# Kernel optimization log

Hardware: AMD Instinct MI355X
Metric: run time of the kernel (lower is better)

## Reference

```python
import jax, jax.numpy as jnp
import numpy as np

B, H, S, D = 1, 32, 2048, 128
LAST_Q = 64      # MInference uses the last 64 queries to estimate the pattern
V_TOPK = 256     # top vertical columns kept per head
S_TOPK = 512     # top slash diagonals kept per head
N_SINK = 4       # vertical columns always kept (attention sink)
N_LOCAL = 64     # local diagonals always kept
SCALE = 1.0 / np.sqrt(D)


def setup_inputs() -> dict:
    key = jax.random.key(0)
    k1, k2, k3 = jax.random.split(key, 3)
    q = jax.random.normal(k1, (B, H, S, D), jnp.float32)
    k = jax.random.normal(k2, (B, H, S, D), jnp.float32)
    v = jax.random.normal(k3, (B, H, S, D), jnp.float32)
    return {"q": q, "k": k, "v": v}


def _vertical_slash_masks(q, k):
    """Estimate per-head vertical/slash importance from the last LAST_Q queries
    and return boolean column mask [B,H,S] and diagonal mask [B,H,S]."""
    ql = q[:, :, -LAST_Q:, :]                                   # [B,H,LQ,D]
    est = jnp.einsum('bhqd,bhkd->bhqk', ql, k) * SCALE          # [B,H,LQ,S]
    rows = jnp.arange(S - LAST_Q, S)                            # global row ids
    cols = jnp.arange(S)
    causal = rows[:, None] >= cols[None, :]                     # [LQ,S]
    est = jnp.where(causal, est, -jnp.inf)
    p = jax.nn.softmax(est, axis=-1)                            # [B,H,LQ,S]

    # vertical importance: column sums of estimated attention
    vertical = p.sum(axis=2)                                    # [B,H,S]

    # slash importance: sums along diagonals d = row - col (d in [0, S-1])
    diag = jnp.clip(rows[:, None] - cols[None, :], 0, S - 1)    # negatives are causally masked (p=0)
    flat_d = diag.reshape(-1)
    flat_p = p.reshape(B * H, LAST_Q * S)
    slash = jax.vmap(lambda pr: jax.ops.segment_sum(pr, flat_d, num_segments=S))(flat_p)
    slash = slash.reshape(B, H, S)                              # [B,H,S]

    # always keep sink columns and the local diagonal band
    vertical = vertical.at[..., :N_SINK].set(jnp.inf)
    slash = slash.at[..., :N_LOCAL].set(jnp.inf)

    _, v_idx = jax.lax.top_k(vertical, V_TOPK)                  # [B,H,V_TOPK]
    _, s_idx = jax.lax.top_k(slash, S_TOPK)                     # [B,H,S_TOPK]

    scatter_true = jax.vmap(jax.vmap(lambda m, i: m.at[i].set(True)))
    vmask = scatter_true(jnp.zeros((B, H, S), bool), v_idx)     # which columns kept
    smask = scatter_true(jnp.zeros((B, H, S), bool), s_idx)     # which diagonals kept
    return vmask, smask


def reference(q, k, v):
    vmask, smask = _vertical_slash_masks(q, k)

    rows = jnp.arange(S)
    cols = jnp.arange(S)
    causal = rows[:, None] >= cols[None, :]                     # [S,S]
    d = jnp.clip(rows[:, None] - cols[None, :], 0, S - 1)       # [S,S] diagonal id

    # keep (r,c) if causal AND (column c is a top vertical OR diagonal r-c is a top slash)
    keep = causal[None, None] & (vmask[:, :, None, :] | jnp.take(smask, d, axis=-1))

    scores = jnp.einsum('bhqd,bhkd->bhqk', q, k) * SCALE        # [B,H,S,S]
    scores = jnp.where(keep, scores, -jnp.inf)
    probs = jax.nn.softmax(scores, axis=-1)                     # every row keeps diagonal 0 -> no all-masked rows
    return jnp.einsum('bhqk,bhkd->bhqd', probs, v)
```

## Files before the change

### kernel.cpp

```cpp
#include <hip/hip_runtime.h>
#include <hip/hip_bf16.h>

#define S_LEN 2048
#define NH 32
#define D_DIM 128
#define LAST_Q 64
#define SCALE_F 0.08838834764831845f
#define QSCALE (0.08838834764831845f * 1.4426950408889634f)
#define RESCALE_THR 11.54f

typedef __attribute__((ext_vector_type(8))) short bf16x8;
typedef __attribute__((ext_vector_type(4))) float f32x4;
typedef unsigned long long u64;
typedef unsigned int u32;
typedef unsigned short u16;

static __device__ __forceinline__ u16 f32_bf16(float f) {
  u32 u = __float_as_uint(f);
  u32 r = (u + 0x7FFFu + ((u >> 16) & 1u)) >> 16;
  return (u16)r;
}

static __device__ __forceinline__ u32 cvt_pk_bf16(float lo, float hi) {
  u32 r;
  asm("v_cvt_pk_bf16_f32 %0, %1, %2" : "=v"(r) : "v"(lo), "v"(hi));
  return r;
}

__global__ __launch_bounds__(256) void conv_kernel(const float* __restrict__ k,
                                                   const float* __restrict__ v,
                                                   u16* __restrict__ kpre,
                                                   u16* __restrict__ vpre) {
  int bid = blockIdx.x;
  int t = bid & 31, h = bid >> 5;
  int tid = threadIdx.x;
  int c0 = t * 64;
  __shared__ u16 Vb[64][136];
  for (int i = tid; i < 512; i += 256) {
    int r = i >> 3, s = i & 7;
    const float* srcp = v + ((size_t)(h * S_LEN + c0 + r)) * D_DIM + s * 16;
    float4 f0 = *(const float4*)(srcp);
    float4 f1 = *(const float4*)(srcp + 4);
    float4 f2 = *(const float4*)(srcp + 8);
    float4 f3 = *(const float4*)(srcp + 12);
    bf16x8 t0, t1;
    t0[0] = (short)f32_bf16(f0.x); t0[1] = (short)f32_bf16(f0.y);
    t0[2] = (short)f32_bf16(f0.z); t0[3] = (short)f32_bf16(f0.w);
    t0[4] = (short)f32_bf16(f1.x); t0[5] = (short)f32_bf16(f1.y);
    t0[6] = (short)f32_bf16(f1.z); t0[7] = (short)f32_bf16(f1.w);
    t1[0] = (short)f32_bf16(f2.x); t1[1] = (short)f32_bf16(f2.y);
    t1[2] = (short)f32_bf16(f2.z); t1[3] = (short)f32_bf16(f2.w);
    t1[4] = (short)f32_bf16(f3.x); t1[5] = (short)f32_bf16(f3.y);
    t1[6] = (short)f32_bf16(f3.z); t1[7] = (short)f32_bf16(f3.w);
    *(bf16x8*)&Vb[r][s * 16] = t0;
    *(bf16x8*)&Vb[r][s * 16 + 8] = t1;
  }
  u16* kp = kpre + (size_t)h * 262144 + (size_t)t * 8192;
#pragma unroll
  for (int j = 0; j < 4; ++j) {
    int p = j * 256 + tid;
    int r = p >> 4;
    int g = (p & 15) ^ (r & 15);
    const float* srcp = k + ((size_t)(h * S_LEN + c0 + r)) * D_DIM + g * 8;
    float4 a = *(const float4*)srcp;
    float4 b = *(const float4*)(srcp + 4);
    bf16x8 o;
    o[0] = (short)f32_bf16(a.x); o[1] = (short)f32_bf16(a.y);
    o[2] = (short)f32_bf16(a.z); o[3] = (short)f32_bf16(a.w);
    o[4] = (short)f32_bf16(b.x); o[5] = (short)f32_bf16(b.y);
    o[6] = (short)f32_bf16(b.z); o[7] = (short)f32_bf16(b.w);
    *(bf16x8*)(kp + p * 8) = o;
  }
  __syncthreads();
  u16* vp = vpre + (size_t)h * 262144 + (size_t)t * 8192;
#pragma unroll
  for (int j = 0; j < 4; ++j) {
    int p = j * 256 + tid;
    int d = p >> 3;
    int cb = (p & 7) ^ (d & 7);
    bf16x8 g;
#pragma unroll
    for (int e = 0; e < 8; ++e) g[e] = (short)Vb[cb * 8 + e][d];
    *(bf16x8*)(vp + p * 8) = g;
  }
}

__global__ __launch_bounds__(256) void est_kernel(const float* __restrict__ q,
                                                  const float* __restrict__ k,
                                                  float* __restrict__ scores) {
  int cc = blockIdx.x;
  int h = blockIdx.y;
  int tid = threadIdx.x;
  int ty = tid >> 4, tx = tid & 15;
  __shared__ float Qs[64][36];
  __shared__ float Ks[64][36];
  float acc[4][4];
#pragma unroll
  for (int i = 0; i < 4; ++i)
#pragma unroll
    for (int j = 0; j < 4; ++j) acc[i][j] = 0.f;
  const float* qbase = q + ((size_t)h * S_LEN + (S_LEN - LAST_Q)) * D_DIM;
  const float* kbase = k + ((size_t)h * S_LEN + cc * 64) * D_DIM;
  for (int dc = 0; dc < 4; ++dc) {
    __syncthreads();
    for (int i = tid; i < 512; i += 256) {
      int r = i >> 3, s = i & 7;
      float4 a = *(const float4*)(qbase + (size_t)r * D_DIM + dc * 32 + s * 4);
      *(float4*)&Qs[r][s * 4] = a;
      float4 b = *(const float4*)(kbase + (size_t)r * D_DIM + dc * 32 + s * 4);
      *(float4*)&Ks[r][s * 4] = b;
    }
    __syncthreads();
#pragma unroll
    for (int d4 = 0; d4 < 8; ++d4) {
      float4 qv[4], kv[4];
#pragma unroll
      for (int i = 0; i < 4; ++i) qv[i] = *(const float4*)&Qs[ty + 16 * i][d4 * 4];
#pragma unroll
      for (int j = 0; j < 4; ++j) kv[j] = *(const float4*)&Ks[tx + 16 * j][d4 * 4];
#pragma unroll
      for (int i = 0; i < 4; ++i)
#pragma unroll
        for (int j = 0; j < 4; ++j)
          acc[i][j] += qv[i].x * kv[j].x + qv[i].y * kv[j].y + qv[i].z * kv[j].z + qv[i].w * kv[j].w;
    }
  }
#pragma unroll
  for (int i = 0; i < 4; ++i) {
    int rl = ty + 16 * i;
    int rg = (S_LEN - LAST_Q) + rl;
#pragma unroll
    for (int j = 0; j < 4; ++j) {
      int cg = cc * 64 + tx + 16 * j;
      float vv = (cg <= rg) ? acc[i][j] * SCALE_F : -1e30f;
      scores[((size_t)h * LAST_Q + rl) * S_LEN + cg] = vv;
    }
  }
}

__global__ __launch_bounds__(256) void soft_partial_kernel(const float* __restrict__ scores,
                                                           float* __restrict__ part) {
  int h = blockIdx.x, rg = blockIdx.y;
  int tid = threadIdx.x;
  int wave = tid >> 6, lane = tid & 63;
  __shared__ float vs[2048];
  __shared__ float ss[2048];
  __shared__ float red[4];
  int i0 = tid * 8;
#pragma unroll
  for (int e = 0; e < 8; ++e) { vs[i0 + e] = 0.f; ss[i0 + e] = 0.f; }
  for (int rr = 0; rr < 8; ++rr) {
    int r = rg * 8 + rr;
    const float* sp = scores + ((size_t)h * LAST_Q + r) * S_LEN;
    float4 a = *(const float4*)(sp + i0);
    float4 b = *(const float4*)(sp + i0 + 4);
    float x[8] = {a.x, a.y, a.z, a.w, b.x, b.y, b.z, b.w};
    float wm = -1e30f;
#pragma unroll
    for (int e = 0; e < 8; ++e) wm = fmaxf(wm, x[e]);
#pragma unroll
    for (int mk = 1; mk < 64; mk <<= 1) wm = fmaxf(wm, __shfl_xor(wm, mk, 64));
    __syncthreads();
    if (lane == 0) red[wave] = wm;
    __syncthreads();
    float m = fmaxf(fmaxf(red[0], red[1]), fmaxf(red[2], red[3]));
    float psum = 0.f;
#pragma unroll
    for (int e = 0; e < 8; ++e) { x[e] = __expf(x[e] - m); psum += x[e]; }
#pragma unroll
    for (int mk = 1; mk < 64; mk <<= 1) psum += __shfl_xor(psum, mk, 64);
    __syncthreads();
    if (lane == 0) red[wave] = psum;
    __syncthreads();
    float inv = 1.f / (red[0] + red[1] + red[2] + red[3]);
    int rgl = (S_LEN - LAST_Q) + r;
#pragma unroll
    for (int e = 0; e < 8; ++e) {
      float p = x[e] * inv;
      int i = i0 + e;
      vs[i] += p;
      int d = rgl - i;
      if (d >= 0) ss[d] += p;
    }
  }
  __syncthreads();
  float* pb = part + ((size_t)(h * 8 + rg)) * 4096;
#pragma unroll
  for (int e = 0; e < 8; ++e) { pb[i0 + e] = vs[i0 + e]; pb[2048 + i0 + e] = ss[i0 + e]; }
}

__global__ __launch_bounds__(256) void topk_kernel(const float* __restrict__ part,
                                                   u64* __restrict__ vbits,
                                                   u64* __restrict__ sbits) {
  int h = blockIdx.x;
  int which = blockIdx.y;
  u64* dst = which ? (sbits + h * 32) : (vbits + h * 32);
  u32 K = which ? 512u : 256u;
  int ninf = which ? 64 : 4;
  int tid = threadIdx.x;
  int lane = tid & 63, wid = tid >> 6;
  __shared__ u32 keys[2048];
  __shared__ u32 hist[256];
  __shared__ u32 wpart[4];
  __shared__ u32 sh_pref, sh_kth;
  __shared__ u64 mbw[32];
  int i0 = tid * 8;
  float accv[8] = {0.f, 0.f, 0.f, 0.f, 0.f, 0.f, 0.f, 0.f};
  for (int rg = 0; rg < 8; ++rg) {
    const float* pp = part + ((size_t)(h * 8 + rg)) * 4096 + which * 2048 + i0;
    float4 a = *(const float4*)pp;
    float4 b = *(const float4*)(pp + 4);
    accv[0] += a.x; accv[1] += a.y; accv[2] += a.z; accv[3] += a.w;
    accv[4] += b.x; accv[5] += b.y; accv[6] += b.z; accv[7] += b.w;
  }
#pragma unroll
  for (int e = 0; e < 8; ++e) {
    int i = i0 + e;
    keys[i] = (i < ninf) ? 0x7F800000u : __float_as_uint(accv[e]);
  }
  __syncthreads();
  u32 prefix = 0;
  u32 kth = K;
  for (int shift = 24; shift >= 0; shift -= 8) {
    hist[tid] = 0;
    __syncthreads();
#pragma unroll
    for (int e = 0; e < 8; ++e) {
      u32 kk = keys[i0 + e];
      if (shift == 24 || (kk >> (shift + 8)) == (prefix >> (shift + 8)))
        atomicAdd(&hist[(kk >> shift) & 255], 1u);
    }
    __syncthreads();
    u32 v = hist[tid];
    u32 x = v;
#pragma unroll
    for (int off = 1; off < 64; off <<= 1) {
      u32 o = __shfl_up(x, off, 64);
      if (lane >= off) x += o;
    }
    if (lane == 63) wpart[wid] = x;
    __syncthreads();
    u32 base = 0;
    for (int w2 = 0; w2 < wid; ++w2) base += wpart[w2];
    u32 T = wpart[0] + wpart[1] + wpart[2] + wpart[3];
    u32 Pincl = x + base;
    u32 Sb = T - Pincl + v;
    u32 Sn = T - Pincl;
    if (Sb >= kth && Sn < kth) {
      sh_pref = prefix | ((u32)tid << shift);
      sh_kth = kth - Sn;
    }
    __syncthreads();
    prefix = sh_pref;
    kth = sh_kth;
    __syncthreads();
  }
  u32 t = prefix;
  u32 cnt = 0;
#pragma unroll
  for (int e = 0; e < 8; ++e) cnt += (keys[i0 + e] == t) ? 1u : 0u;
  u32 x = cnt;
#pragma unroll
  for (int off = 1; off < 64; off <<= 1) {
    u32 o = __shfl_up(x, off, 64);
    if (lane >= off) x += o;
  }
  if (lane == 63) wpart[wid] = x;
  __syncthreads();
  u32 base = 0;
  for (int w2 = 0; w2 < wid; ++w2) base += wpart[w2];
  u32 exc = x + base - cnt;
  unsigned char myb = 0;
  u32 seen = 0;
#pragma unroll
  for (int e = 0; e < 8; ++e) {
    u32 kk = keys[i0 + e];
    bool in = (kk > t) || (kk == t && (exc + seen) < kth);
    if (kk == t) ++seen;
    myb |= (in ? 1u : 0u) << e;
  }
  ((unsigned char*)mbw)[tid] = myb;
  __syncthreads();
  if (tid < 32) dst[tid] = mbw[tid];
}

template <bool PRE>
__global__ __launch_bounds__(256, 4) void attn_kernel(const float* __restrict__ q,
                                                      const float* __restrict__ kk,
                                                      const float* __restrict__ vv,
                                                      const u16* __restrict__ kpre,
                                                      const u16* __restrict__ vpre,
                                                      const u64* __restrict__ vbits,
                                                      const u64* __restrict__ sbits,
                                                      float* __restrict__ out) {
  int bid = blockIdx.x;
  int u = bid & 255, s = bid >> 8;
  int h = u & 31;
  int v_ = u >> 5;
  int qt;
  switch (s) {
    case 0: qt = v_; break;
    case 1: qt = 31 - v_; break;
    case 2: qt = v_ + 16; break;
    default: qt = 15 - v_; break;
  }
  int tid = threadIdx.x;
  int wave = tid >> 6, lane = tid & 63;
  int grp = lane >> 4, ln = lane & 15;

  __shared__ u16 Ks[8192];
  __shared__ u16 Vt[8192];
  __shared__ u64 smp[34];

  if (tid < 34) smp[tid] = (tid == 0 || tid == 33) ? 0ull : sbits[h * 32 + tid - 1];

  int q0w = qt * 64 + wave * 16;
  bf16x8 qf[4];
  const float* qrow = q + ((size_t)h * S_LEN + q0w + ln) * D_DIM;
#pragma unroll
  for (int ks = 0; ks < 4; ++ks) {
    const float* p = qrow + ks * 32 + grp * 8;
    float4 a = *(const float4*)p;
    float4 b = *(const float4*)(p + 4);
    bf16x8 f;
    f[0] = (short)f32_bf16(a.x * QSCALE); f[1] = (short)f32_bf16(a.y * QSCALE);
    f[2] = (short)f32_bf16(a.z * QSCALE); f[3] = (short)f32_bf16(a.w * QSCALE);
    f[4] = (short)f32_bf16(b.x * QSCALE); f[5] = (short)f32_bf16(b.y * QSCALE);
    f[6] = (short)f32_bf16(b.z * QSCALE); f[7] = (short)f32_bf16(b.w * QSCALE);
    qf[ks] = f;
  }
  f32x4 of[8];
#pragma unroll
  for (int i = 0; i < 8; ++i) of[i] = (f32x4){0.f, 0.f, 0.f, 0.f};
  float mr = -1e30f;
  float ls = 0.f;

  const int kb0 = (ln << 7) + (((0 + grp) ^ ln) << 3);
  const int kb1 = (ln << 7) + (((4 + grp) ^ ln) << 3);
  const int kb2 = (ln << 7) + (((8 + grp) ^ ln) << 3);
  const int kb3 = (ln << 7) + (((12 + grp) ^ ln) << 3);
  const int vb0 = (ln << 6) + (((0 + grp) ^ (ln & 7)) << 3);
  const int vb1 = (ln << 6) + (((4 + grp) ^ (ln & 7)) << 3);

  const u16* kp = kpre + (size_t)h * 262144;
  const u16* vp = vpre + (size_t)h * 262144;
  const float* kfb = kk + (size_t)h * S_LEN * D_DIM;
  const float* vfb = vv + (size_t)h * S_LEN * D_DIM;
  const u64* vwp = vbits + h * 32;
  int nt = qt + 1;
  int sb_lane = (lane & 48) + ((lane & 48) >> 2);

  auto dma_k = [&](int t) {
    const u16* ksrc = kp + (size_t)t * 8192;
#pragma unroll
    for (int i = 0; i < 4; ++i) {
      int chunk = wave * 4 + i;
      __builtin_amdgcn_global_load_lds(
          (const __attribute__((address_space(1))) u32*)(const void*)(ksrc + (size_t)(chunk * 64 + lane) * 8),
          (__attribute__((address_space(3))) u32*)(void*)(&Ks[chunk * 512]), 16, 0, 0);
    }
  };
  auto dma_v = [&](int t) {
    const u16* vsrc = vp + (size_t)t * 8192;
#pragma unroll
    for (int i = 0; i < 4; ++i) {
      int chunk = wave * 4 + i;
      __builtin_amdgcn_global_load_lds(
          (const __attribute__((address_space(1))) u32*)(const void*)(vsrc + (size_t)(chunk * 64 + lane) * 8),
          (__attribute__((address_space(3))) u32*)(void*)(&Vt[chunk * 512]), 16, 0, 0);
    }
  };

  if constexpr (PRE) { dma_k(0); dma_v(0); }
  __syncthreads();

  for (int t = 0; t < nt; ++t) {
    int c0 = t * 64;
    if constexpr (!PRE) {
      for (int i = tid; i < 512; i += 256) {
        int r = i >> 3, s2 = i & 7;
        const float* srcp = kfb + (size_t)(c0 + r) * D_DIM + s2 * 16;
        float4 f0 = *(const float4*)(srcp);
        float4 f1 = *(const float4*)(srcp + 4);
        float4 f2 = *(const float4*)(srcp + 8);
        float4 f3 = *(const float4*)(srcp + 12);
        bf16x8 t0, t1;
        t0[0] = (short)f32_bf16(f0.x); t0[1] = (short)f32_bf16(f0.y);
        t0[2] = (short)f32_bf16(f0.z); t0[3] = (short)f32_bf16(f0.w);
        t0[4] = (short)f32_bf16(f1.x); t0[5] = (short)f32_bf16(f1.y);
        t0[6] = (short)f32_bf16(f1.z); t0[7] = (short)f32_bf16(f1.w);
        t1[0] = (short)f32_bf16(f2.x); t1[1] = (short)f32_bf16(f2.y);
        t1[2] = (short)f32_bf16(f2.z); t1[3] = (short)f32_bf16(f2.w);
        t1[4] = (short)f32_bf16(f3.x); t1[5] = (short)f32_bf16(f3.y);
        t1[6] = (short)f32_bf16(f3.z); t1[7] = (short)f32_bf16(f3.w);
        int cb0 = s2 * 2, cb1 = s2 * 2 + 1;
        *(bf16x8*)&Ks[r * 128 + ((cb0 ^ (r & 15)) << 3)] = t0;
        *(bf16x8*)&Ks[r * 128 + ((cb1 ^ (r & 15)) << 3)] = t1;
      }
      for (int i = tid; i < 512; i += 256) {
        int r = i >> 3, s2 = i & 7;
        const float* srcp = vfb + (size_t)(c0 + r) * D_DIM + s2 * 16;
#pragma unroll
        for (int x = 0; x < 16; x += 4) {
          float4 f4 = *(const float4*)(srcp + x);
          int d0 = s2 * 16 + x;
          float vals[4] = {f4.x, f4.y, f4.z, f4.w};
#pragma unroll
          for (int y = 0; y < 4; ++y) {
            int d = d0 + y;
            Vt[d * 64 + (((r >> 3) ^ (d & 7)) << 3) + (r & 7)] = f32_bf16(vals[y]);
          }
        }
      }
      __syncthreads();
    }

    f32x4 sfr[4];
#pragma unroll
    for (int nb = 0; nb < 4; ++nb) {
      f32x4 acc = (f32x4){0.f, 0.f, 0.f, 0.f};
      acc = __builtin_amdgcn_mfma_f32_16x16x32_bf16(*(const bf16x8*)&Ks[kb0 + nb * 2048], qf[0], acc, 0, 0, 0);
      acc = __builtin_amdgcn_mfma_f32_16x16x32_bf16(*(const bf16x8*)&Ks[kb1 + nb * 2048], qf[1], acc, 0, 0, 0);
      acc = __builtin_amdgcn_mfma_f32_16x16x32_bf16(*(const bf16x8*)&Ks[kb2 + nb * 2048], qf[2], acc, 0, 0, 0);
      acc = __builtin_amdgcn_mfma_f32_16x16x32_bf16(*(const bf16x8*)&Ks[kb3 + nb * 2048], qf[3], acc, 0, 0, 0);
      sfr[nb] = acc;
    }

    float tm = sfr[0][0];
#pragma unroll
    for (int nb = 0; nb < 4; ++nb)
#pragma unroll
      for (int jj = 0; jj < 4; ++jj) tm = fmaxf(tm, sfr[nb][jj]);
    tm = fmaxf(tm, __shfl_xor(tm, 16, 64));
    tm = fmaxf(tm, __shfl_xor(tm, 32, 64));

    if (__any(tm - mr > RESCALE_THR)) {
      float mn = fmaxf(mr, tm);
      float ex = __builtin_amdgcn_exp2f(mr - mn);
      mr = mn;
      ls *= ex;
      float e0 = __shfl(ex, sb_lane, 64);
      float e1 = __shfl(ex, sb_lane + 1, 64);
      float e2 = __shfl(ex, sb_lane + 2, 64);
      float e3 = __shfl(ex, sb_lane + 3, 64);
#pragma unroll
      for (int db = 0; db < 8; ++db) {
        of[db][0] *= e0; of[db][1] *= e1; of[db][2] *= e2; of[db][3] *= e3;
      }
    }

    int Cb = (q0w + ln) - c0 - (grp << 2);
    float rs = 0.f;
    u32 pkw[8];
    if (c0 >= q0w - 48) {
#pragma unroll
      for (int nb = 0; nb < 4; ++nb) {
        float pv[4];
#pragma unroll
        for (int jj = 0; jj < 4; ++jj) {
          bool keep = (16 * nb + jj) <= Cb;
          float p = keep ? __builtin_amdgcn_exp2f(sfr[nb][jj] - mr) : 0.f;
          rs += p;
          pv[jj] = p;
        }
        pkw[nb * 2] = cvt_pk_bf16(pv[0], pv[1]);
        pkw[nb * 2 + 1] = cvt_pk_bf16(pv[2], pv[3]);
      }
    } else {
      int b0 = Cb - 63;
      int w0i = (b0 >> 6) + 1;
      int sh = b0 & 63;
      u64 lo = smp[w0i];
      u64 hi = smp[w0i + 1];
      u64 W = (sh == 0) ? lo : ((lo >> sh) | (hi << (64 - sh)));
      u64 vword = vwp[t];
#pragma unroll
      for (int nb = 0; nb < 4; ++nb) {
        u32 vn = (u32)(vword >> (16 * nb + 4 * grp)) & 0xFu;
        u32 sn = (u32)(W >> (60 - 16 * nb)) & 0xFu;
        float pv[4];
#pragma unroll
        for (int jj = 0; jj < 4; ++jj) {
          u32 keep = ((vn >> jj) | (sn >> (3 - jj))) & 1u;
          float p = keep ? __builtin_amdgcn_exp2f(sfr[nb][jj] - mr) : 0.f;
          rs += p;
          pv[jj] = p;
        }
        pkw[nb * 2] = cvt_pk_bf16(pv[0], pv[1]);
        pkw[nb * 2 + 1] = cvt_pk_bf16(pv[2], pv[3]);
      }
    }
    rs += __shfl_xor(rs, 16, 64);
    rs += __shfl_xor(rs, 32, 64);
    ls += rs;

    if constexpr (PRE) {
      __builtin_amdgcn_sched_barrier(0);
      asm volatile("s_waitcnt vmcnt(0)" ::: "memory");
      __builtin_amdgcn_s_barrier();
      if (t + 1 < nt) dma_k(t + 1);
    }

#pragma unroll
    for (int ks2 = 0; ks2 < 2; ++ks2) {
      int sl0 = ln + ((lane & 16) << 1);
      int sl1 = sl0 + 16;
      u32 a0 = __shfl(pkw[ks2 * 4 + 0], sl0, 64);
      u32 a1 = __shfl(pkw[ks2 * 4 + 1], sl0, 64);
      u32 a2 = __shfl(pkw[ks2 * 4 + 0], sl1, 64);
      u32 a3 = __shfl(pkw[ks2 * 4 + 1], sl1, 64);
      u32 b0_ = __shfl(pkw[ks2 * 4 + 2], sl0, 64);
      u32 b1_ = __shfl(pkw[ks2 * 4 + 3], sl0, 64);
      u32 b2_ = __shfl(pkw[ks2 * 4 + 2], sl1, 64);
      u32 b3_ = __shfl(pkw[ks2 * 4 + 3], sl1, 64);
      bool hi2 = grp >= 2;
      union { u32 w[4]; bf16x8 v; } pu;
      pu.w[0] = hi2 ? b0_ : a0;
      pu.w[1] = hi2 ? b1_ : a1;
      pu.w[2] = hi2 ? b2_ : a2;
      pu.w[3] = hi2 ? b3_ : a3;
      int vb = ks2 ? vb1 : vb0;
#pragma unroll
      for (int db = 0; db < 8; ++db) {
        bf16x8 vf = *(const bf16x8*)&Vt[vb + db * 1024];
        of[db] = __builtin_amdgcn_mfma_f32_16x16x32_bf16(pu.v, vf, of[db], 0, 0, 0);
      }
    }

    if constexpr (PRE) {
      __builtin_amdgcn_sched_barrier(0);
      __builtin_amdgcn_s_barrier();
      if (t + 1 < nt) {
        dma_v(t + 1);
        asm volatile("s_waitcnt vmcnt(4)" ::: "memory");
      }
      __builtin_amdgcn_s_barrier();
    } else {
      __syncthreads();
    }
  }

  float invl = 1.f / ls;
  float i0 = __shfl(invl, sb_lane, 64);
  float i1 = __shfl(invl, sb_lane + 1, 64);
  float i2 = __shfl(invl, sb_lane + 2, 64);
  float i3 = __shfl(invl, sb_lane + 3, 64);
  float* ob = out + ((size_t)h * S_LEN + q0w) * D_DIM;
#pragma unroll
  for (int db = 0; db < 8; ++db) {
    ob[(size_t)(grp * 4 + 0) * D_DIM + db * 16 + ln] = of[db][0] * i0;
    ob[(size_t)(grp * 4 + 1) * D_DIM + db * 16 + ln] = of[db][1] * i1;
    ob[(size_t)(grp * 4 + 2) * D_DIM + db * 16 + ln] = of[db][2] * i2;
    ob[(size_t)(grp * 4 + 3) * D_DIM + db * 16 + ln] = of[db][3] * i3;
  }
}

extern "C" void kernel_launch(void* const* d_in, const int* in_sizes, int n_in,
                              void* d_out, int out_size, void* d_ws, size_t ws_size,
                              hipStream_t stream) {
  const float* q = (const float*)d_in[0];
  const float* k = (const float*)d_in[1];
  const float* v = (const float*)d_in[2];
  float* out = (float*)d_out;
  float* scores = out;
  float* part = out + 4194304;
  u64* vbits = (u64*)d_ws;
  u64* sbits = vbits + 1024;
  const size_t PRE_NEED = 16384 + 2ull * 16777216;
  bool pre = ws_size >= PRE_NEED;
  u16* kpre = (u16*)((char*)d_ws + 16384);
  u16* vpre = kpre + 8388608;

  if (pre) conv_kernel<<<1024, 256, 0, stream>>>(k, v, kpre, vpre);
  est_kernel<<<dim3(32, 32), 256, 0, stream>>>(q, k, scores);
  soft_partial_kernel<<<dim3(32, 8), 256, 0, stream>>>(scores, part);
  topk_kernel<<<dim3(32, 2), 256, 0, stream>>>(part, vbits, sbits);
  if (pre)
    attn_kernel<true><<<1024, 256, 0, stream>>>(q, k, v, kpre, vpre, vbits, sbits, out);
  else
    attn_kernel<false><<<1024, 256, 0, stream>>>(q, k, v, kpre, vpre, vbits, sbits, out);
}
```

Measured before the change: 140.9 us.

## Pair causal query tiles per block, fuse conversion with estimation, split softmax partials

The attention kernel now gives each block two query tiles (qt and 31-qt). Each K/V tile staged in shared memory is used by both, which halves the block count and balances causal work across blocks. Conversion and estimation are merged into one launch by interleaving block roles. The softmax-partial kernel uses 16 row groups instead of 8 for more parallelism, and top-k reduces the extra partials. Occupancy hints drop to 2 blocks per CU because of the doubled register state (two accumulators and two Q fragments), and setprio hints are added around the MFMA sections.

```diff
diff --git a/kernel.cpp b/kernel.cpp
--- a/kernel.cpp
+++ b/kernel.cpp
@@ -27,61 +27,114 @@
   return r;
 }
 
-__global__ __launch_bounds__(256) void conv_kernel(const float* __restrict__ k,
-                                                   const float* __restrict__ v,
-                                                   u16* __restrict__ kpre,
-                                                   u16* __restrict__ vpre) {
+__global__ __launch_bounds__(256) void conv_est_kernel(const float* __restrict__ k,
+                                                       const float* __restrict__ v,
+                                                       const float* __restrict__ q,
+                                                       u16* __restrict__ kpre,
+                                                       u16* __restrict__ vpre,
+                                                       float* __restrict__ scores) {
+  __shared__ char smem[18432];
   int bid = blockIdx.x;
-  int t = bid & 31, h = bid >> 5;
+  int b = bid >> 1;
   int tid = threadIdx.x;
-  int c0 = t * 64;
-  __shared__ u16 Vb[64][136];
-  for (int i = tid; i < 512; i += 256) {
-    int r = i >> 3, s = i & 7;
-    const float* srcp = v + ((size_t)(h * S_LEN + c0 + r)) * D_DIM + s * 16;
-    float4 f0 = *(const float4*)(srcp);
-    float4 f1 = *(const float4*)(srcp + 4);
-    float4 f2 = *(const float4*)(srcp + 8);
-    float4 f3 = *(const float4*)(srcp + 12);
-    bf16x8 t0, t1;
-    t0[0] = (short)f32_bf16(f0.x); t0[1] = (short)f32_bf16(f0.y);
-    t0[2] = (short)f32_bf16(f0.z); t0[3] = (short)f32_bf16(f0.w);
-    t0[4] = (short)f32_bf16(f1.x); t0[5] = (short)f32_bf16(f1.y);
-    t0[6] = (short)f32_bf16(f1.z); t0[7] = (short)f32_bf16(f1.w);
-    t1[0] = (short)f32_bf16(f2.x); t1[1] = (short)f32_bf16(f2.y);
-    t1[2] = (short)f32_bf16(f2.z); t1[3] = (short)f32_bf16(f2.w);
-    t1[4] = (short)f32_bf16(f3.x); t1[5] = (short)f32_bf16(f3.y);
-    t1[6] = (short)f32_bf16(f3.z); t1[7] = (short)f32_bf16(f3.w);
-    *(bf16x8*)&Vb[r][s * 16] = t0;
-    *(bf16x8*)&Vb[r][s * 16 + 8] = t1;
-  }
-  u16* kp = kpre + (size_t)h * 262144 + (size_t)t * 8192;
-#pragma unroll
-  for (int j = 0; j < 4; ++j) {
-    int p = j * 256 + tid;
-    int r = p >> 4;
-    int g = (p & 15) ^ (r & 15);
-    const float* srcp = k + ((size_t)(h * S_LEN + c0 + r)) * D_DIM + g * 8;
-    float4 a = *(const float4*)srcp;
-    float4 b = *(const float4*)(srcp + 4);
-    bf16x8 o;
-    o[0] = (short)f32_bf16(a.x); o[1] = (short)f32_bf16(a.y);
-    o[2] = (short)f32_bf16(a.z); o[3] = (short)f32_bf16(a.w);
-    o[4] = (short)f32_bf16(b.x); o[5] = (short)f32_bf16(b.y);
-    o[6] = (short)f32_bf16(b.z); o[7] = (short)f32_bf16(b.w);
-    *(bf16x8*)(kp + p * 8) = o;
-  }
-  __syncthreads();
-  u16* vp = vpre + (size_t)h * 262144 + (size_t)t * 8192;
-#pragma unroll
-  for (int j = 0; j < 4; ++j) {
-    int p = j * 256 + tid;
-    int d = p >> 3;
-    int cb = (p & 7) ^ (d & 7);
-    bf16x8 g;
-#pragma unroll
-    for (int e = 0; e < 8; ++e) g[e] = (short)Vb[cb * 8 + e][d];
-    *(bf16x8*)(vp + p * 8) = g;
+  if ((bid & 1) == 0) {
+    int t = b & 31, h = b >> 5;
+    int c0 = t * 64;
+    u16 (*Vb)[136] = (u16(*)[136])smem;
+    for (int i = tid; i < 512; i += 256) {
+      int r = i >> 3, s = i & 7;
+      const float* srcp = v + ((size_t)(h * S_LEN + c0 + r)) * D_DIM + s * 16;
+      float4 f0 = *(const float4*)(srcp);
+      float4 f1 = *(const float4*)(srcp + 4);
+      float4 f2 = *(const float4*)(srcp + 8);
+      float4 f3 = *(const float4*)(srcp + 12);
+      bf16x8 t0, t1;
+      t0[0] = (short)f32_bf16(f0.x); t0[1] = (short)f32_bf16(f0.y);
+      t0[2] = (short)f32_bf16(f0.z); t0[3] = (short)f32_bf16(f0.w);
+      t0[4] = (short)f32_bf16(f1.x); t0[5] = (short)f32_bf16(f1.y);
+      t0[6] = (short)f32_bf16(f1.z); t0[7] = (short)f32_bf16(f1.w);
+      t1[0] = (short)f32_bf16(f2.x); t1[1] = (short)f32_bf16(f2.y);
+      t1[2] = (short)f32_bf16(f2.z); t1[3] = (short)f32_bf16(f2.w);
+      t1[4] = (short)f32_bf16(f3.x); t1[5] = (short)f32_bf16(f3.y);
+      t1[6] = (short)f32_bf16(f3.z); t1[7] = (short)f32_bf16(f3.w);
+      *(bf16x8*)&Vb[r][s * 16] = t0;
+      *(bf16x8*)&Vb[r][s * 16 + 8] = t1;
+    }
+    u16* kp = kpre + (size_t)h * 262144 + (size_t)t * 8192;
+#pragma unroll
+    for (int j = 0; j < 4; ++j) {
+      int p = j * 256 + tid;
+      int r = p >> 4;
+      int g = (p & 15) ^ (r & 15);
+      const float* srcp = k + ((size_t)(h * S_LEN + c0 + r)) * D_DIM + g * 8;
+      float4 a = *(const float4*)srcp;
+      float4 bb = *(const float4*)(srcp + 4);
+      bf16x8 o;
+      o[0] = (short)f32_bf16(a.x); o[1] = (short)f32_bf16(a.y);
+      o[2] = (short)f32_bf16(a.z); o[3] = (short)f32_bf16(a.w);
+      o[4] = (short)f32_bf16(bb.x); o[5] = (short)f32_bf16(bb.y);
+      o[6] = (short)f32_bf16(bb.z); o[7] = (short)f32_bf16(bb.w);
+      *(bf16x8*)(kp + p * 8) = o;
+    }
+    __syncthreads();
+    u16* vp = vpre + (size_t)h * 262144 + (size_t)t * 8192;
+#pragma unroll
+    for (int j = 0; j < 4; ++j) {
+      int p = j * 256 + tid;
+      int d = p >> 3;
+      int cb = (p & 7) ^ (d & 7);
+      bf16x8 g;
+#pragma unroll
+      for (int e = 0; e < 8; ++e) g[e] = (short)Vb[cb * 8 + e][d];
+      *(bf16x8*)(vp + p * 8) = g;
+    }
+  } else {
+    int cc = b & 31, h = b >> 5;
+    float (*Qs)[36] = (float(*)[36])smem;
+    float (*Ks)[36] = (float(*)[36])(smem + 9216);
+    int ty = tid >> 4, tx = tid & 15;
+    float acc[4][4];
+#pragma unroll
+    for (int i = 0; i < 4; ++i)
+#pragma unroll
+      for (int j = 0; j < 4; ++j) acc[i][j] = 0.f;
+    const float* qbase = q + ((size_t)h * S_LEN + (S_LEN - LAST_Q)) * D_DIM;
+    const float* kbase = k + ((size_t)h * S_LEN + cc * 64) * D_DIM;
+    for (int dc = 0; dc < 4; ++dc) {
+      __syncthreads();
+      for (int i = tid; i < 512; i += 256) {
+        int r = i >> 3, s = i & 7;
+        float4 a = *(const float4*)(qbase + (size_t)r * D_DIM + dc * 32 + s * 4);
+        *(float4*)&Qs[r][s * 4] = a;
+        float4 bb = *(const float4*)(kbase + (size_t)r * D_DIM + dc * 32 + s * 4);
+        *(float4*)&Ks[r][s * 4] = bb;
+      }
+      __syncthreads();
+#pragma unroll
+      for (int d4 = 0; d4 < 8; ++d4) {
+        float4 qv[4], kv[4];
+#pragma unroll
+        for (int i = 0; i < 4; ++i) qv[i] = *(const float4*)&Qs[ty + 16 * i][d4 * 4];
+#pragma unroll
+        for (int j = 0; j < 4; ++j) kv[j] = *(const float4*)&Ks[tx + 16 * j][d4 * 4];
+#pragma unroll
+        for (int i = 0; i < 4; ++i)
+#pragma unroll
+          for (int j = 0; j < 4; ++j)
+            acc[i][j] += qv[i].x * kv[j].x + qv[i].y * kv[j].y + qv[i].z * kv[j].z + qv[i].w * kv[j].w;
+      }
+    }
+#pragma unroll
+    for (int i = 0; i < 4; ++i) {
+      int rl = ty + 16 * i;
+      int rg = (S_LEN - LAST_Q) + rl;
+#pragma unroll
+      for (int j = 0; j < 4; ++j) {
+        int cg = cc * 64 + tx + 16 * j;
+        float vv = (cg <= rg) ? acc[i][j] * SCALE_F : -1e30f;
+        scores[((size_t)h * LAST_Q + rl) * S_LEN + cg] = vv;
+      }
+    }
   }
 }
 
@@ -149,8 +202,8 @@
   int i0 = tid * 8;
 #pragma unroll
   for (int e = 0; e < 8; ++e) { vs[i0 + e] = 0.f; ss[i0 + e] = 0.f; }
-  for (int rr = 0; rr < 8; ++rr) {
-    int r = rg * 8 + rr;
+  for (int rr = 0; rr < 4; ++rr) {
+    int r = rg * 4 + rr;
     const float* sp = scores + ((size_t)h * LAST_Q + r) * S_LEN;
     float4 a = *(const float4*)(sp + i0);
     float4 b = *(const float4*)(sp + i0 + 4);
@@ -184,7 +237,7 @@
     }
   }
   __syncthreads();
-  float* pb = part + ((size_t)(h * 8 + rg)) * 4096;
+  float* pb = part + ((size_t)(h * 16 + rg)) * 4096;
 #pragma unroll
   for (int e = 0; e < 8; ++e) { pb[i0 + e] = vs[i0 + e]; pb[2048 + i0 + e] = ss[i0 + e]; }
 }
@@ -206,8 +259,8 @@
   __shared__ u64 mbw[32];
   int i0 = tid * 8;
   float accv[8] = {0.f, 0.f, 0.f, 0.f, 0.f, 0.f, 0.f, 0.f};
-  for (int rg = 0; rg < 8; ++rg) {
-    const float* pp = part + ((size_t)(h * 8 + rg)) * 4096 + which * 2048 + i0;
+  for (int rg = 0; rg < 16; ++rg) {
+    const float* pp = part + ((size_t)(h * 16 + rg)) * 4096 + which * 2048 + i0;
     float4 a = *(const float4*)pp;
     float4 b = *(const float4*)(pp + 4);
     accv[0] += a.x; accv[1] += a.y; accv[2] += a.z; accv[3] += a.w;
@@ -285,7 +338,7 @@
 }
 
 template <bool PRE>
-__global__ __launch_bounds__(256, 4) void attn_kernel(const float* __restrict__ q,
+__global__ __launch_bounds__(256, 2) void attn_kernel(const float* __restrict__ q,
                                                       const float* __restrict__ kk,
                                                       const float* __restrict__ vv,
                                                       const u16* __restrict__ kpre,
@@ -294,16 +347,10 @@
                                                       const u64* __restrict__ sbits,
                                                       float* __restrict__ out) {
   int bid = blockIdx.x;
-  int u = bid & 255, s = bid >> 8;
+  int u = bid & 255;
   int h = u & 31;
-  int v_ = u >> 5;
-  int qt;
-  switch (s) {
-    case 0: qt = v_; break;
-    case 1: qt = 31 - v_; break;
-    case 2: qt = v_ + 16; break;
-    default: qt = 15 - v_; break;
-  }
+  int idx = ((u >> 5) & 7) + ((bid >> 8) << 3);
+  int qtA = idx, qtB = 31 - idx;
   int tid = threadIdx.x;
   int wave = tid >> 6, lane = tid & 63;
   int grp = lane >> 4, ln = lane & 15;
@@ -314,26 +361,42 @@
 
   if (tid < 34) smp[tid] = (tid == 0 || tid == 33) ? 0ull : sbits[h * 32 + tid - 1];
 
-  int q0w = qt * 64 + wave * 16;
-  bf16x8 qf[4];
-  const float* qrow = q + ((size_t)h * S_LEN + q0w + ln) * D_DIM;
-#pragma unroll
-  for (int ks = 0; ks < 4; ++ks) {
-    const float* p = qrow + ks * 32 + grp * 8;
-    float4 a = *(const float4*)p;
-    float4 b = *(const float4*)(p + 4);
-    bf16x8 f;
-    f[0] = (short)f32_bf16(a.x * QSCALE); f[1] = (short)f32_bf16(a.y * QSCALE);
-    f[2] = (short)f32_bf16(a.z * QSCALE); f[3] = (short)f32_bf16(a.w * QSCALE);
-    f[4] = (short)f32_bf16(b.x * QSCALE); f[5] = (short)f32_bf16(b.y * QSCALE);
-    f[6] = (short)f32_bf16(b.z * QSCALE); f[7] = (short)f32_bf16(b.w * QSCALE);
-    qf[ks] = f;
-  }
-  f32x4 of[8];
-#pragma unroll
-  for (int i = 0; i < 8; ++i) of[i] = (f32x4){0.f, 0.f, 0.f, 0.f};
-  float mr = -1e30f;
-  float ls = 0.f;
+  int q0A = qtA * 64 + wave * 16;
+  int q0B = qtB * 64 + wave * 16;
+
+  bf16x8 qfA[4], qfB[4];
+  {
+    const float* qrowA = q + ((size_t)h * S_LEN + q0A + ln) * D_DIM;
+    const float* qrowB = q + ((size_t)h * S_LEN + q0B + ln) * D_DIM;
+#pragma unroll
+    for (int ks = 0; ks < 4; ++ks) {
+      const float* pA = qrowA + ks * 32 + grp * 8;
+      const float* pB = qrowB + ks * 32 + grp * 8;
+      float4 a = *(const float4*)pA;
+      float4 b = *(const float4*)(pA + 4);
+      bf16x8 f;
+      f[0] = (short)f32_bf16(a.x * QSCALE); f[1] = (short)f32_bf16(a.y * QSCALE);
+      f[2] = (short)f32_bf16(a.z * QSCALE); f[3] = (short)f32_bf16(a.w * QSCALE);
+      f[4] = (short)f32_bf16(b.x * QSCALE); f[5] = (short)f32_bf16(b.y * QSCALE);
+      f[6] = (short)f32_bf16(b.z * QSCALE); f[7] = (short)f32_bf16(b.w * QSCALE);
+      qfA[ks] = f;
+      a = *(const float4*)pB;
+      b = *(const float4*)(pB + 4);
+      f[0] = (short)f32_bf16(a.x * QSCALE); f[1] = (short)f32_bf16(a.y * QSCALE);
+      f[2] = (short)f32_bf16(a.z * QSCALE); f[3] = (short)f32_bf16(a.w * QSCALE);
+      f[4] = (short)f32_bf16(b.x * QSCALE); f[5] = (short)f32_bf16(b.y * QSCALE);
+      f[6] = (short)f32_bf16(b.z * QSCALE); f[7] = (short)f32_bf16(b.w * QSCALE);
+      qfB[ks] = f;
+    }
+  }
+  f32x4 ofA[8], ofB[8];
+#pragma unroll
+  for (int i = 0; i < 8; ++i) {
+    ofA[i] = (f32x4){0.f, 0.f, 0.f, 0.f};
+    ofB[i] = (f32x4){0.f, 0.f, 0.f, 0.f};
+  }
+  float mrA = -1e30f, lsA = 0.f;
+  float mrB = -1e30f, lsB = 0.f;
 
   const int kb0 = (ln << 7) + (((0 + grp) ^ ln) << 3);
   const int kb1 = (ln << 7) + (((4 + grp) ^ ln) << 3);
@@ -347,7 +410,7 @@
   const float* kfb = kk + (size_t)h * S_LEN * D_DIM;
   const float* vfb = vv + (size_t)h * S_LEN * D_DIM;
   const u64* vwp = vbits + h * 32;
-  int nt = qt + 1;
+  int nt = qtB + 1;
   int sb_lane = (lane & 48) + ((lane & 48) >> 2);
 
   auto dma_k = [&](int t) {
@@ -368,6 +431,115 @@
       __builtin_amdgcn_global_load_lds(
           (const __attribute__((address_space(1))) u32*)(const void*)(vsrc + (size_t)(chunk * 64 + lane) * 8),
           (__attribute__((address_space(3))) u32*)(void*)(&Vt[chunk * 512]), 16, 0, 0);
+    }
+  };
+
+  auto qk_sm = [&](int c0, int q0w, const bf16x8* qf, f32x4* of, float& mr, float& ls,
+                   u32* pkw, u64 vword) {
+    f32x4 sfr[4];
+    __builtin_amdgcn_s_setprio(1);
+#pragma unroll
+    for (int nb = 0; nb < 4; ++nb) {
+      f32x4 acc = (f32x4){0.f, 0.f, 0.f, 0.f};
+      acc = __builtin_amdgcn_mfma_f32_16x16x32_bf16(*(const bf16x8*)&Ks[kb0 + nb * 2048], qf[0], acc, 0, 0, 0);
+      acc = __builtin_amdgcn_mfma_f32_16x16x32_bf16(*(const bf16x8*)&Ks[kb1 + nb * 2048], qf[1], acc, 0, 0, 0);
+      acc = __builtin_amdgcn_mfma_f32_16x16x32_bf16(*(const bf16x8*)&Ks[kb2 + nb * 2048], qf[2], acc, 0, 0, 0);
+      acc = __builtin_amdgcn_mfma_f32_16x16x32_bf16(*(const bf16x8*)&Ks[kb3 + nb * 2048], qf[3], acc, 0, 0, 0);
+      sfr[nb] = acc;
+    }
+    __builtin_amdgcn_s_setprio(0);
+    float tm = sfr[0][0];
+#pragma unroll
+    for (int nb = 0; nb < 4; ++nb)
+#pragma unroll
+      for (int jj = 0; jj < 4; ++jj) tm = fmaxf(tm, sfr[nb][jj]);
+    tm = fmaxf(tm, __shfl_xor(tm, 16, 64));
+    tm = fmaxf(tm, __shfl_xor(tm, 32, 64));
+    if (__any(tm - mr > RESCALE_THR)) {
+      float mn = fmaxf(mr, tm);
+      float ex = __builtin_amdgcn_exp2f(mr - mn);
+      mr = mn;
+      ls *= ex;
+      float e0 = __shfl(ex, sb_lane, 64);
+      float e1 = __shfl(ex, sb_lane + 1, 64);
+      float e2 = __shfl(ex, sb_lane + 2, 64);
+      float e3 = __shfl(ex, sb_lane + 3, 64);
+#pragma unroll
+      for (int db = 0; db < 8; ++db) {
+        of[db][0] *= e0; of[db][1] *= e1; of[db][2] *= e2; of[db][3] *= e3;
+      }
+    }
+    int Cb = (q0w + ln) - c0 - (grp << 2);
+    float rs = 0.f;
+    if (c0 >= q0w - 48) {
+#pragma unroll
+      for (int nb = 0; nb < 4; ++nb) {
+        float pv[4];
+#pragma unroll
+        for (int jj = 0; jj < 4; ++jj) {
+          bool keep = (16 * nb + jj) <= Cb;
+          float p = keep ? __builtin_amdgcn_exp2f(sfr[nb][jj] - mr) : 0.f;
+          rs += p;
+          pv[jj] = p;
+        }
+        pkw[nb * 2] = cvt_pk_bf16(pv[0], pv[1]);
+        pkw[nb * 2 + 1] = cvt_pk_bf16(pv[2], pv[3]);
+      }
+    } else {
+      int b0 = Cb - 63;
+      int w0i = (b0 >> 6) + 1;
+      int sh = b0 & 63;
+      u64 lo = smp[w0i];
+      u64 hi = smp[w0i + 1];
+      u64 W = (sh == 0) ? lo : ((lo >> sh) | (hi << (64 - sh)));
+#pragma unroll
+      for (int nb = 0; nb < 4; ++nb) {
+        u32 vn = (u32)(vword >> (16 * nb + 4 * grp)) & 0xFu;
+        u32 sn = (u32)(W >> (60 - 16 * nb)) & 0xFu;
+        float pv[4];
+#pragma unroll
+        for (int jj = 0; jj < 4; ++jj) {
+          u32 keep = ((vn >> jj) | (sn >> (3 - jj))) & 1u;
+          float p = keep ? __builtin_amdgcn_exp2f(sfr[nb][jj] - mr) : 0.f;
+          rs += p;
+          pv[jj] = p;
+        }
+        pkw[nb * 2] = cvt_pk_bf16(pv[0], pv[1]);
+        pkw[nb * 2 + 1] = cvt_pk_bf16(pv[2], pv[3]);
+      }
+    }
+    rs += __shfl_xor(rs, 16, 64);
+    rs += __shfl_xor(rs, 32, 64);
+    ls += rs;
+  };
+
+  auto pv_phase = [&](const u32* pkw, f32x4* of) {
+#pragma unroll
+    for (int ks2 = 0; ks2 < 2; ++ks2) {
+      int sl0 = ln + ((lane & 16) << 1);
+      int sl1 = sl0 + 16;
+      u32 a0 = __shfl(pkw[ks2 * 4 + 0], sl0, 64);
+      u32 a1 = __shfl(pkw[ks2 * 4 + 1], sl0, 64);
+      u32 a2 = __shfl(pkw[ks2 * 4 + 0], sl1, 64);
+      u32 a3 = __shfl(pkw[ks2 * 4 + 1], sl1, 64);
+      u32 b0_ = __shfl(pkw[ks2 * 4 + 2], sl0, 64);
+      u32 b1_ = __shfl(pkw[ks2 * 4 + 3], sl0, 64);
+      u32 b2_ = __shfl(pkw[ks2 * 4 + 2], sl1, 64);
+      u32 b3_ = __shfl(pkw[ks2 * 4 + 3], sl1, 64);
+      bool hi2 = grp >= 2;
+      union { u32 w[4]; bf16x8 v; } pu;
+      pu.w[0] = hi2 ? b0_ : a0;
+      pu.w[1] = hi2 ? b1_ : a1;
+      pu.w[2] = hi2 ? b2_ : a2;
+      pu.w[3] = hi2 ? b3_ : a3;
+      int vb = ks2 ? vb1 : vb0;
+      __builtin_amdgcn_s_setprio(1);
+#pragma unroll
+      for (int db = 0; db < 8; ++db) {
+        bf16x8 vf = *(const bf16x8*)&Vt[vb + db * 1024];
+        of[db] = __builtin_amdgcn_mfma_f32_16x16x32_bf16(pu.v, vf, of[db], 0, 0, 0);
+      }
+      __builtin_amdgcn_s_setprio(0);
     }
   };
 
@@ -415,84 +587,11 @@
       __syncthreads();
     }
 
-    f32x4 sfr[4];
-#pragma unroll
-    for (int nb = 0; nb < 4; ++nb) {
-      f32x4 acc = (f32x4){0.f, 0.f, 0.f, 0.f};
-      acc = __builtin_amdgcn_mfma_f32_16x16x32_bf16(*(const bf16x8*)&Ks[kb0 + nb * 2048], qf[0], acc, 0, 0, 0);
-      acc = __builtin_amdgcn_mfma_f32_16x16x32_bf16(*(const bf16x8*)&Ks[kb1 + nb * 2048], qf[1], acc, 0, 0, 0);
-      acc = __builtin_amdgcn_mfma_f32_16x16x32_bf16(*(const bf16x8*)&Ks[kb2 + nb * 2048], qf[2], acc, 0, 0, 0);
-      acc = __builtin_amdgcn_mfma_f32_16x16x32_bf16(*(const bf16x8*)&Ks[kb3 + nb * 2048], qf[3], acc, 0, 0, 0);
-      sfr[nb] = acc;
-    }
-
-    float tm = sfr[0][0];
-#pragma unroll
-    for (int nb = 0; nb < 4; ++nb)
-#pragma unroll
-      for (int jj = 0; jj < 4; ++jj) tm = fmaxf(tm, sfr[nb][jj]);
-    tm = fmaxf(tm, __shfl_xor(tm, 16, 64));
-    tm = fmaxf(tm, __shfl_xor(tm, 32, 64));
-
-    if (__any(tm - mr > RESCALE_THR)) {
-      float mn = fmaxf(mr, tm);
-      float ex = __builtin_amdgcn_exp2f(mr - mn);
-      mr = mn;
-      ls *= ex;
-      float e0 = __shfl(ex, sb_lane, 64);
-      float e1 = __shfl(ex, sb_lane + 1, 64);
-      float e2 = __shfl(ex, sb_lane + 2, 64);
-      float e3 = __shfl(ex, sb_lane + 3, 64);
-#pragma unroll
-      for (int db = 0; db < 8; ++db) {
-        of[db][0] *= e0; of[db][1] *= e1; of[db][2] *= e2; of[db][3] *= e3;
-      }
-    }
-
-    int Cb = (q0w + ln) - c0 - (grp << 2);
-    float rs = 0.f;
-    u32 pkw[8];
-    if (c0 >= q0w - 48) {
-#pragma unroll
-      for (int nb = 0; nb < 4; ++nb) {
-        float pv[4];
-#pragma unroll
-        for (int jj = 0; jj < 4; ++jj) {
-          bool keep = (16 * nb + jj) <= Cb;
-          float p = keep ? __builtin_amdgcn_exp2f(sfr[nb][jj] - mr) : 0.f;
-          rs += p;
-          pv[jj] = p;
-        }
-        pkw[nb * 2] = cvt_pk_bf16(pv[0], pv[1]);
-        pkw[nb * 2 + 1] = cvt_pk_bf16(pv[2], pv[3]);
-      }
-    } else {
-      int b0 = Cb - 63;
-      int w0i = (b0 >> 6) + 1;
-      int sh = b0 & 63;
-      u64 lo = smp[w0i];
-      u64 hi = smp[w0i + 1];
-      u64 W = (sh == 0) ? lo : ((lo >> sh) | (hi << (64 - sh)));
-      u64 vword = vwp[t];
-#pragma unroll
-      for (int nb = 0; nb < 4; ++nb) {
-        u32 vn = (u32)(vword >> (16 * nb + 4 * grp)) & 0xFu;
-        u32 sn = (u32)(W >> (60 - 16 * nb)) & 0xFu;
-        float pv[4];
-#pragma unroll
-        for (int jj = 0; jj < 4; ++jj) {
-          u32 keep = ((vn >> jj) | (sn >> (3 - jj))) & 1u;
-          float p = keep ? __builtin_amdgcn_exp2f(sfr[nb][jj] - mr) : 0.f;
-          rs += p;
-          pv[jj] = p;
-        }
-        pkw[nb * 2] = cvt_pk_bf16(pv[0], pv[1]);
-        pkw[nb * 2 + 1] = cvt_pk_bf16(pv[2], pv[3]);
-      }
-    }
-    rs += __shfl_xor(rs, 16, 64);
-    rs += __shfl_xor(rs, 32, 64);
-    ls += rs;
+    u64 vword = vwp[t];
+    bool doA = (t <= qtA);
+    u32 pkwB[8], pkwA[8];
+    qk_sm(c0, q0B, qfB, ofB, mrB, lsB, pkwB, vword);
+    if (doA) qk_sm(c0, q0A, qfA, ofA, mrA, lsA, pkwA, vword);
 
     if constexpr (PRE) {
       __builtin_amdgcn_sched_barrier(0);
@@ -501,31 +600,8 @@
       if (t + 1 < nt) dma_k(t + 1);
     }
 
-#pragma unroll
-    for (int ks2 = 0; ks2 < 2; ++ks2) {
-      int sl0 = ln + ((lane & 16) << 1);
-      int sl1 = sl0 + 16;
-      u32 a0 = __shfl(pkw[ks2 * 4 + 0], sl0, 64);
-      u32 a1 = __shfl(pkw[ks2 * 4 + 1], sl0, 64);
-      u32 a2 = __shfl(pkw[ks2 * 4 + 0], sl1, 64);
-      u32 a3 = __shfl(pkw[ks2 * 4 + 1], sl1, 64);
-      u32 b0_ = __shfl(pkw[ks2 * 4 + 2], sl0, 64);
-      u32 b1_ = __shfl(pkw[ks2 * 4 + 3], sl0, 64);
-      u32 b2_ = __shfl(pkw[ks2 * 4 + 2], sl1, 64);
-      u32 b3_ = __shfl(pkw[ks2 * 4 + 3], sl1, 64);
-      bool hi2 = grp >= 2;
-      union { u32 w[4]; bf16x8 v; } pu;
-      pu.w[0] = hi2 ? b0_ : a0;
-      pu.w[1] = hi2 ? b1_ : a1;
-      pu.w[2] = hi2 ? b2_ : a2;
-      pu.w[3] = hi2 ? b3_ : a3;
-      int vb = ks2 ? vb1 : vb0;
-#pragma unroll
-      for (int db = 0; db < 8; ++db) {
-        bf16x8 vf = *(const bf16x8*)&Vt[vb + db * 1024];
-        of[db] = __builtin_amdgcn_mfma_f32_16x16x32_bf16(pu.v, vf, of[db], 0, 0, 0);
-      }
-    }
+    pv_phase(pkwB, ofB);
+    if (doA) pv_phase(pkwA, ofA);
 
     if constexpr (PRE) {
       __builtin_amdgcn_sched_barrier(0);
@@ -540,18 +616,28 @@
     }
   }
 
-  float invl = 1.f / ls;
-  float i0 = __shfl(invl, sb_lane, 64);
-  float i1 = __shfl(invl, sb_lane + 1, 64);
-  float i2 = __shfl(invl, sb_lane + 2, 64);
-  float i3 = __shfl(invl, sb_lane + 3, 64);
-  float* ob = out + ((size_t)h * S_LEN + q0w) * D_DIM;
+  float invA = 1.f / lsA;
+  float invB = 1.f / lsB;
+  float a0 = __shfl(invA, sb_lane, 64);
+  float a1 = __shfl(invA, sb_lane + 1, 64);
+  float a2 = __shfl(invA, sb_lane + 2, 64);
+  float a3 = __shfl(invA, sb_lane + 3, 64);
+  float b0 = __shfl(invB, sb_lane, 64);
+  float b1 = __shfl(invB, sb_lane + 1, 64);
+  float b2 = __shfl(invB, sb_lane + 2, 64);
+  float b3 = __shfl(invB, sb_lane + 3, 64);
+  float* obA = out + ((size_t)h * S_LEN + q0A) * D_DIM;
+  float* obB = out + ((size_t)h * S_LEN + q0B) * D_DIM;
 #pragma unroll
   for (int db = 0; db < 8; ++db) {
-    ob[(size_t)(grp * 4 + 0) * D_DIM + db * 16 + ln] = of[db][0] * i0;
-    ob[(size_t)(grp * 4 + 1) * D_DIM + db * 16 + ln] = of[db][1] * i1;
-    ob[(size_t)(grp * 4 + 2) * D_DIM + db * 16 + ln] = of[db][2] * i2;
-    ob[(size_t)(grp * 4 + 3) * D_DIM + db * 16 + ln] = of[db][3] * i3;
+    obA[(size_t)(grp * 4 + 0) * D_DIM + db * 16 + ln] = ofA[db][0] * a0;
+    obA[(size_t)(grp * 4 + 1) * D_DIM + db * 16 + ln] = ofA[db][1] * a1;
+    obA[(size_t)(grp * 4 + 2) * D_DIM + db * 16 + ln] = ofA[db][2] * a2;
+    obA[(size_t)(grp * 4 + 3) * D_DIM + db * 16 + ln] = ofA[db][3] * a3;
+    obB[(size_t)(grp * 4 + 0) * D_DIM + db * 16 + ln] = ofB[db][0] * b0;
+    obB[(size_t)(grp * 4 + 1) * D_DIM + db * 16 + ln] = ofB[db][1] * b1;
+    obB[(size_t)(grp * 4 + 2) * D_DIM + db * 16 + ln] = ofB[db][2] * b2;
+    obB[(size_t)(grp * 4 + 3) * D_DIM + db * 16 + ln] = ofB[db][3] * b3;
   }
 }
 
@@ -571,12 +657,15 @@
   u16* kpre = (u16*)((char*)d_ws + 16384);
   u16* vpre = kpre + 8388608;
 
-  if (pre) conv_kernel<<<1024, 256, 0, stream>>>(k, v, kpre, vpre);
-  est_kernel<<<dim3(32, 32), 256, 0, stream>>>(q, k, scores);
-  soft_partial_kernel<<<dim3(32, 8), 256, 0, stream>>>(scores, part);
+  if (pre) {
+    conv_est_kernel<<<2048, 256, 0, stream>>>(k, v, q, kpre, vpre, scores);
+  } else {
+    est_kernel<<<dim3(32, 32), 256, 0, stream>>>(q, k, scores);
+  }
+  soft_partial_kernel<<<dim3(32, 16), 256, 0, stream>>>(scores, part);
   topk_kernel<<<dim3(32, 2), 256, 0, stream>>>(part, vbits, sbits);
   if (pre)
-    attn_kernel<true><<<1024, 256, 0, stream>>>(q, k, v, kpre, vpre, vbits, sbits, out);
+    attn_kernel<true><<<512, 256, 0, stream>>>(q, k, v, kpre, vpre, vbits, sbits, out);
   else
-    attn_kernel<false><<<1024, 256, 0, stream>>>(q, k, v, kpre, vpre, vbits, sbits, out);
-}
+    attn_kernel<false><<<512, 256, 0, stream>>>(q, k, v, kpre, vpre, vbits, sbits, out);
+}
```

After: 149.3 us. +6.0%, slower.
